# Kernel optimization log

Measured on AMD Instinct MI355X. Metric: run time of the kernel, lower is better.

Reference implementation:

```python
import jax, jax.numpy as jnp
import numpy as np

WS = 8
NUM_HEADS = 8
EMBED_DIM = 256
LN_EPS = 1e-5


def setup_inputs() -> dict:
    key = jax.random.key(0)
    ks = jax.random.split(key, 5)
    b, c, h, w = 4, EMBED_DIM, 128, 128
    return {
        "x": jax.random.normal(ks[0], (b, c, h, w), dtype=jnp.float32),
        "in_proj_w": jax.random.normal(ks[1], (3 * c, c), dtype=jnp.float32) * 0.02,
        "in_proj_b": jax.random.normal(ks[2], (3 * c,), dtype=jnp.float32) * 0.02,
        "out_w": jax.random.normal(ks[3], (c, c), dtype=jnp.float32) * 0.02,
        "out_b": jax.random.normal(ks[4], (c,), dtype=jnp.float32) * 0.02,
        "ln_w": jnp.ones((c,), dtype=jnp.float32),
        "ln_b": jnp.zeros((c,), dtype=jnp.float32),
    }


def reference(x, in_proj_w, in_proj_b, out_w, out_b, ln_w, ln_b):
    b, c, h, w = x.shape
    pad_h = (-h) % WS
    pad_w = (-w) % WS
    xp = jnp.pad(x, ((0, 0), (0, 0), (0, pad_h), (0, pad_w)))
    Hp, Wp = h + pad_h, w + pad_w
    h1, w1 = Hp // WS, Wp // WS
    L = h1 * w1            # attention sequence = number of windows
    N = b * WS * WS        # attention batch = b * within-window positions
    # rearrange 'b c (h1 h2) (w1 w2) -> (h1 w1) (b h2 w2) c', then batch-first
    t = xp.reshape(b, c, h1, WS, w1, WS)
    t = jnp.transpose(t, (2, 4, 0, 3, 5, 1)).reshape(L, N, c)
    t = jnp.transpose(t, (1, 0, 2))  # [N, L, c]
    # nn.MultiheadAttention (self-attention, no mask)
    qkv = t @ in_proj_w.T + in_proj_b  # [N, L, 3c]
    q, k, v = jnp.split(qkv, 3, axis=-1)
    D = c // NUM_HEADS
    q = q.reshape(N, L, NUM_HEADS, D) * (D ** -0.5)
    k = k.reshape(N, L, NUM_HEADS, D)
    v = v.reshape(N, L, NUM_HEADS, D)
    attn = jax.nn.softmax(jnp.einsum('nlhd,nmhd->nhlm', q, k), axis=-1)
    o = jnp.einsum('nhlm,nmhd->nlhd', attn, v).reshape(N, L, c)
    o = o @ out_w.T + out_b
    # LayerNorm over channel dim
    mu = jnp.mean(o, axis=-1, keepdims=True)
    var = jnp.mean(jnp.square(o - mu), axis=-1, keepdims=True)
    o = (o - mu) * jax.lax.rsqrt(var + LN_EPS) * ln_w + ln_b
    # inverse rearrange '(h1 w1) (b h2 w2) c -> b c (h1 h2) (w1 w2)'
    y = jnp.transpose(o, (1, 0, 2)).reshape(h1, w1, b, WS, WS, c)
    y = jnp.transpose(y, (2, 5, 0, 3, 1, 4)).reshape(b, c, Hp, Wp)
    return y[:, :, :h, :w]
```

## Files before the change

kernel.cpp:

```cpp
#include <hip/hip_runtime.h>
#include <stdint.h>
#include <stddef.h>


typedef __attribute__((ext_vector_type(8))) short bf16x8;
typedef __attribute__((ext_vector_type(4))) float f32x4;
typedef __attribute__((ext_vector_type(16))) float f32x16;
typedef __attribute__((ext_vector_type(4))) unsigned u32x4;
typedef __attribute__((ext_vector_type(2))) unsigned u32x2;
typedef unsigned short bf16u;

#define LOG2E 1.4426950408889634f
#define MFMA32(a, b, c) __builtin_amdgcn_mfma_f32_32x32x16_bf16(a, b, c, 0, 0, 0)

__device__ __forceinline__ bf16u f2b(float f) {
  uint32_t u = __float_as_uint(f);
  u += 0x7fffu + ((u >> 16) & 1u);
  return (bf16u)(u >> 16);
}
__device__ __forceinline__ float b2f(bf16u s) {
  return __uint_as_float(((uint32_t)s) << 16);
}

__device__ __forceinline__ void gload_lds16(const void* g, void* l) {
  __builtin_amdgcn_global_load_lds((__attribute__((address_space(1))) void*)(g),
                                   (__attribute__((address_space(3))) void*)(l),
                                   16, 0, 0);
}

__device__ __forceinline__ unsigned cvtpk(float a, float b) {
  unsigned r;
  asm("v_cvt_pk_bf16_f32 %0, %1, %2" : "=v"(r) : "v"(a), "v"(b));
  return r;
}

__device__ __forceinline__ void swap32(unsigned a, unsigned b, bool hi,
                                       unsigned& x, unsigned& y) {
#if __has_builtin(__builtin_amdgcn_permlane32_swap)
  typedef __attribute__((ext_vector_type(2))) unsigned uint2v;
  uint2v r = __builtin_amdgcn_permlane32_swap(a, b, false, false);
  x = r.x;
  y = r.y;
#else
  unsigned as = (unsigned)__shfl_xor((int)a, 32);
  unsigned bs = (unsigned)__shfl_xor((int)b, 32);
  x = hi ? bs : a;
  y = hi ? b : as;
#endif
}

__global__ __launch_bounds__(256) void k_convert(const float* __restrict__ s,
                                                 bf16u* __restrict__ d, int n) {
  int i = blockIdx.x * 256 + threadIdx.x;
  if (i < n) d[i] = f2b(s[i]);
}

__global__ __launch_bounds__(256) void k_rearrange(const float* __restrict__ x,
                                                   bf16u* __restrict__ Tb) {
  const int bid = blockIdx.x;
  const int ct = bid & 7, hh = (bid >> 3) & 127, b = bid >> 10;
  const int c0 = ct * 32;
  const int h1 = hh >> 3, h2 = hh & 7;
  __shared__ float tile[32][129];
  for (int e = threadIdx.x; e < 4096; e += 256) {
    int cc = e >> 7, ww = e & 127;
    tile[cc][ww] = x[(((size_t)(b * 256 + c0 + cc)) * 128 + hh) * 128 + ww];
  }
  __syncthreads();
  for (int e = threadIdx.x; e < 4096; e += 256) {
    int ww = e >> 5, cc = e & 31;
    int w1 = ww >> 3, w2 = ww & 7;
    int i = ((b * 64 + h2 * 8 + w2) << 8) | (h1 * 16 + w1);
    Tb[(size_t)i * 256 + c0 + cc] = f2b(tile[cc][ww]);
  }
}

__global__ __launch_bounds__(256) void k_qkv(const bf16u* __restrict__ Tb,
                                             const bf16u* __restrict__ Wb,
                                             const float* __restrict__ bias,
                                             bf16u* __restrict__ Qb,
                                             bf16u* __restrict__ Kb,
                                             bf16u* __restrict__ Vtb) {
  __shared__ bf16u As[128 * 64];
  __shared__ bf16u Bs[128 * 64];
  const int bid0 = blockIdx.x;
  const int bid = (bid0 & 7) * 384 + (bid0 >> 3);
  const int o0 = (bid % 6) * 128;
  const int i0 = (bid / 6) * 128;
  const int seg = o0 >> 8;
  const int t = threadIdx.x;
  const int lane = t & 63, lo = lane & 15, hi = lane >> 4;
  const int w = t >> 6, wr = w >> 1, wc = w & 1;
  const int rr = t >> 3, cc8 = t & 7;
  f32x4 acc[4][4] = {};
  for (int k0 = 0; k0 < 256; k0 += 64) {
    __syncthreads();
#pragma unroll
    for (int j = 0; j < 4; ++j) {
      const int row = j * 32 + rr;
      const int sc = (cc8 ^ (row & 7)) * 8;
      bf16u* const da = As + (j * 32 + w * 8) * 64;
      bf16u* const db = Bs + (j * 32 + w * 8) * 64;
      gload_lds16(Tb + (size_t)(i0 + row) * 256 + k0 + sc, da);
      gload_lds16(Wb + (size_t)(o0 + row) * 256 + k0 + sc, db);
    }
    __syncthreads();
#pragma unroll
    for (int ks = 0; ks < 2; ++ks) {
      bf16x8 af[4], bf_[4];
#pragma unroll
      for (int m = 0; m < 4; ++m) {
        const int row = wr * 64 + m * 16 + lo;
        const int c = (ks * 4 + hi) ^ (lo & 7);
        af[m] = *(const bf16x8*)&As[row * 64 + c * 8];
      }
#pragma unroll
      for (int nn = 0; nn < 4; ++nn) {
        const int row = wc * 64 + nn * 16 + lo;
        const int c = (ks * 4 + hi) ^ (lo & 7);
        bf_[nn] = *(const bf16x8*)&Bs[row * 64 + c * 8];
      }
#pragma unroll
      for (int m = 0; m < 4; ++m)
#pragma unroll
        for (int nn = 0; nn < 4; ++nn)
          acc[m][nn] = __builtin_amdgcn_mfma_f32_16x16x32_bf16(af[m], bf_[nn], acc[m][nn], 0, 0, 0);
    }
  }
  const float oscale = (seg == 0) ? (0.17677669529663687f * LOG2E) : 1.0f;
#pragma unroll
  for (int m = 0; m < 4; ++m) {
#pragma unroll
    for (int nn = 0; nn < 4; ++nn) {
      const int o = o0 + wc * 64 + nn * 16 + lo;
      const int within = o & 255, head = within >> 5, dd = within & 31;
      const float bia = bias[o];
      const int tok0 = i0 + wr * 64 + m * 16 + hi * 4;
      const int nt = tok0 >> 8, ls0 = tok0 & 255;
      if (seg == 2) {
        float v0 = acc[m][nn][0] + bia, v1 = acc[m][nn][1] + bia;
        float v2 = acc[m][nn][2] + bia, v3 = acc[m][nn][3] + bia;
        u32x2 pkd = {cvtpk(v0, v1), cvtpk(v2, v3)};
        *(u32x2*)(Vtb + ((size_t)((nt * 8 + head) * 32 + dd)) * 256 + ls0) = pkd;
      } else {
        bf16u* const dst = (seg == 0) ? Qb : Kb;
#pragma unroll
        for (int r = 0; r < 4; ++r) {
          float v = (acc[m][nn][r] + bia) * oscale;
          dst[((size_t)((nt * 8 + head) * 256 + ls0 + r)) * 32 + dd] = f2b(v);
        }
      }
    }
  }
}

__global__ __launch_bounds__(256, 2) void k_attn(const bf16u* __restrict__ Qb,
                                                 const bf16u* __restrict__ Kb,
                                                 const bf16u* __restrict__ Vtb,
                                                 bf16u* __restrict__ Ob) {
  const int nh = blockIdx.x;
  const int n = nh >> 3, h = nh & 7;
  const bf16u* Qp = Qb + (size_t)nh * 8192;
  const bf16u* Kp = Kb + (size_t)nh * 8192;
  const bf16u* Vp = Vtb + (size_t)nh * 8192;
  const int t = threadIdx.x, w = t >> 6, lane = t & 63;
  const int l31 = lane & 31;
  const bool hi5 = (lane & 32) != 0;

  bf16x8 qf[2][2];
#pragma unroll
  for (int qs = 0; qs < 2; ++qs)
#pragma unroll
    for (int dh = 0; dh < 2; ++dh)
      qf[qs][dh] = *(const bf16x8*)(Qp + (size_t)(w * 64 + qs * 32 + l31) * 32 +
                                    dh * 16 + (hi5 ? 8 : 0));

  const bf16u* kbase = Kp + (size_t)l31 * 32 + (hi5 ? 8 : 0);
  const bf16u* vbase = Vp + (size_t)l31 * 256 + (hi5 ? 8 : 0);

  bf16x8 kf0 = *(const bf16x8*)(kbase);
  bf16x8 kf1 = *(const bf16x8*)(kbase + 16);
  bf16x8 vf0 = *(const bf16x8*)(vbase);
  bf16x8 vf1 = *(const bf16x8*)(vbase + 16);

  f32x16 accO[2] = {};
  float rsum[2] = {0.f, 0.f};

#pragma unroll
  for (int kt = 0; kt < 8; ++kt) {
    const int nkt = (kt + 1) & 7;
    bf16x8 nk0 = *(const bf16x8*)(kbase + nkt * 1024);
    bf16x8 nk1 = *(const bf16x8*)(kbase + nkt * 1024 + 16);
    bf16x8 nv0 = *(const bf16x8*)(vbase + nkt * 32);
    bf16x8 nv1 = *(const bf16x8*)(vbase + nkt * 32 + 16);

#pragma unroll
    for (int qs = 0; qs < 2; ++qs) {
      f32x16 s = {};
      s = MFMA32(kf0, qf[qs][0], s);
      s = MFMA32(kf1, qf[qs][1], s);
      float ts0 = 0.f, ts1 = 0.f;
      unsigned pk[8];
#pragma unroll
      for (int jp = 0; jp < 8; ++jp) {
        float p0 = exp2f(s[2 * jp]);
        float p1 = exp2f(s[2 * jp + 1]);
        ts0 += p0;
        ts1 += p1;
        pk[jp] = cvtpk(p0, p1);
      }
      float ts = ts0 + ts1;
      ts += __shfl_xor(ts, 32);
      rsum[qs] += ts;
      unsigned x0, x1, x2, x3, y0, y1, y2, y3;
      swap32(pk[0], pk[2], hi5, x0, x2);
      swap32(pk[1], pk[3], hi5, x1, x3);
      swap32(pk[4], pk[6], hi5, y0, y2);
      swap32(pk[5], pk[7], hi5, y1, y3);
      u32x4 pa0 = {x0, x1, x2, x3};
      u32x4 pa1 = {y0, y1, y2, y3};
      accO[qs] = MFMA32(__builtin_bit_cast(bf16x8, pa0), vf0, accO[qs]);
      accO[qs] = MFMA32(__builtin_bit_cast(bf16x8, pa1), vf1, accO[qs]);
    }
    kf0 = nk0;
    kf1 = nk1;
    vf0 = nv0;
    vf1 = nv1;
  }
#pragma unroll
  for (int qs = 0; qs < 2; ++qs) {
    float rn = 1.0f / rsum[qs];
#pragma unroll
    for (int r = 0; r < 16; ++r) {
      int row = (r & 3) + 8 * (r >> 2) + ((lane & 32) >> 3);
      float c = __shfl(rn, (lane & 32) | row);
      float o = accO[qs][r] * c;
      Ob[((size_t)(n * 256 + w * 64 + qs * 32 + row)) * 256 + h * 32 + l31] = f2b(o);
    }
  }
}

__global__ __launch_bounds__(256) void k_out(const bf16u* __restrict__ Ob,
                                             const bf16u* __restrict__ Wb,
                                             const float* __restrict__ bias,
                                             const float* __restrict__ lnw,
                                             const float* __restrict__ lnb,
                                             bf16u* __restrict__ On) {
  __shared__ bf16u As[64 * 64];
  __shared__ bf16u Bs[256 * 64];
  __shared__ float red[64][4][2];
  const int i0 = blockIdx.x * 64;
  const int t = threadIdx.x, w = t >> 6, lane = t & 63, lo = lane & 15, hi = lane >> 4;
  const int rr = t >> 3, cc8 = t & 7;
  f32x4 acc[4][4] = {};
  for (int k0 = 0; k0 < 256; k0 += 64) {
    __syncthreads();
#pragma unroll
    for (int j = 0; j < 2; ++j) {
      const int row = j * 32 + rr;
      const int sc = (cc8 ^ (row & 7)) * 8;
      gload_lds16(Ob + (size_t)(i0 + row) * 256 + k0 + sc,
                  As + (j * 32 + w * 8) * 64);
    }
#pragma unroll
    for (int j = 0; j < 8; ++j) {
      const int row = j * 32 + rr;
      const int sc = (cc8 ^ (row & 7)) * 8;
      gload_lds16(Wb + (size_t)row * 256 + k0 + sc,
                  Bs + (j * 32 + w * 8) * 64);
    }
    __syncthreads();
#pragma unroll
    for (int ks = 0; ks < 2; ++ks) {
      bf16x8 af[4], bf_[4];
#pragma unroll
      for (int m = 0; m < 4; ++m) {
        const int row = m * 16 + lo;
        const int c = (ks * 4 + hi) ^ (lo & 7);
        af[m] = *(const bf16x8*)&As[row * 64 + c * 8];
      }
#pragma unroll
      for (int nn = 0; nn < 4; ++nn) {
        const int row = w * 64 + nn * 16 + lo;
        const int c = (ks * 4 + hi) ^ (lo & 7);
        bf_[nn] = *(const bf16x8*)&Bs[row * 64 + c * 8];
      }
#pragma unroll
      for (int m = 0; m < 4; ++m)
#pragma unroll
        for (int nn = 0; nn < 4; ++nn)
          acc[m][nn] = __builtin_amdgcn_mfma_f32_16x16x32_bf16(af[m], bf_[nn], acc[m][nn], 0, 0, 0);
    }
  }
#pragma unroll
  for (int m = 0; m < 4; ++m)
#pragma unroll
    for (int nn = 0; nn < 4; ++nn) {
      float bia = bias[w * 64 + nn * 16 + lo];
#pragma unroll
      for (int r = 0; r < 4; ++r) acc[m][nn][r] += bia;
    }
#pragma unroll
  for (int m = 0; m < 4; ++m)
#pragma unroll
    for (int r = 0; r < 4; ++r) {
      float sv = acc[m][0][r] + acc[m][1][r] + acc[m][2][r] + acc[m][3][r];
      float sq = acc[m][0][r] * acc[m][0][r] + acc[m][1][r] * acc[m][1][r] +
                 acc[m][2][r] * acc[m][2][r] + acc[m][3][r] * acc[m][3][r];
      sv += __shfl_xor(sv, 1); sq += __shfl_xor(sq, 1);
      sv += __shfl_xor(sv, 2); sq += __shfl_xor(sq, 2);
      sv += __shfl_xor(sv, 4); sq += __shfl_xor(sq, 4);
      sv += __shfl_xor(sv, 8); sq += __shfl_xor(sq, 8);
      if (lo == 0) {
        red[m * 16 + hi * 4 + r][w][0] = sv;
        red[m * 16 + hi * 4 + r][w][1] = sq;
      }
    }
  __syncthreads();
#pragma unroll
  for (int m = 0; m < 4; ++m)
#pragma unroll
    for (int r = 0; r < 4; ++r) {
      int row = m * 16 + hi * 4 + r;
      float S  = red[row][0][0] + red[row][1][0] + red[row][2][0] + red[row][3][0];
      float Q2 = red[row][0][1] + red[row][1][1] + red[row][2][1] + red[row][3][1];
      float mu = S * 0.00390625f;
      float var = Q2 * 0.00390625f - mu * mu;
      float rstd = rsqrtf(var + 1e-5f);
#pragma unroll
      for (int nn = 0; nn < 4; ++nn) {
        int oc = w * 64 + nn * 16 + lo;
        float o = (acc[m][nn][r] - mu) * rstd * lnw[oc] + lnb[oc];
        On[(size_t)(i0 + row) * 256 + oc] = f2b(o);
      }
    }
}

__global__ __launch_bounds__(256) void k_unrearrange(const bf16u* __restrict__ On,
                                                     float* __restrict__ y) {
  const int bid = blockIdx.x;
  const int ct = bid & 7, hh = (bid >> 3) & 127, b = bid >> 10;
  const int c0 = ct * 32;
  const int h1 = hh >> 3, h2 = hh & 7;
  __shared__ float tile[32][129];
  for (int e = threadIdx.x; e < 4096; e += 256) {
    int ww = e >> 5, cc = e & 31;
    int w1 = ww >> 3, w2 = ww & 7;
    int i = ((b * 64 + h2 * 8 + w2) << 8) | (h1 * 16 + w1);
    tile[cc][ww] = b2f(On[(size_t)i * 256 + c0 + cc]);
  }
  __syncthreads();
  for (int e = threadIdx.x; e < 4096; e += 256) {
    int cc = e >> 7, ww = e & 127;
    y[(((size_t)(b * 256 + c0 + cc)) * 128 + hh) * 128 + ww] = tile[cc][ww];
  }
}

extern "C" void kernel_launch(void* const* d_in, const int* in_sizes, int n_in,
                              void* d_out, int out_size, void* d_ws, size_t ws_size,
                              hipStream_t stream) {
  const float* x     = (const float*)d_in[0];
  const float* w_qkv = (const float*)d_in[1];
  const float* b_qkv = (const float*)d_in[2];
  const float* w_out = (const float*)d_in[3];
  const float* b_out = (const float*)d_in[4];
  const float* ln_w  = (const float*)d_in[5];
  const float* ln_b  = (const float*)d_in[6];
  float* y = (float*)d_out;

  const size_t SEG = 33554432;
  char* ws = (char*)d_ws;
  if (ws_size < 5 * SEG + 768 * 256 * 2 + 256 * 256 * 2) return;
  bf16u* Tb = (bf16u*)(ws);
  bf16u* Qb = (bf16u*)(ws + SEG);
  bf16u* Kb = (bf16u*)(ws + 2 * SEG);
  bf16u* Vtb = (bf16u*)(ws + 3 * SEG);
  bf16u* Ob = (bf16u*)(ws + 4 * SEG);
  bf16u* Wqkvb = (bf16u*)(ws + 5 * SEG);
  bf16u* Woutb = (bf16u*)(ws + 5 * SEG + 768 * 256 * 2);
  bf16u* On = Tb;

  k_convert<<<768, 256, 0, stream>>>(w_qkv, Wqkvb, 768 * 256);
  k_convert<<<256, 256, 0, stream>>>(w_out, Woutb, 256 * 256);
  k_rearrange<<<4096, 256, 0, stream>>>(x, Tb);
  k_qkv<<<3072, 256, 0, stream>>>(Tb, Wqkvb, b_qkv, Qb, Kb, Vtb);
  k_attn<<<2048, 256, 0, stream>>>(Qb, Kb, Vtb, Ob);
  k_out<<<1024, 256, 0, stream>>>(Ob, Woutb, b_out, ln_w, ln_b, On);
  k_unrearrange<<<4096, 256, 0, stream>>>(On, y);
}
```

Measured before the change: 179.9 us.

## Stage K and V tiles in swizzled LDS for attention kernel

The attention kernel now copies the whole per-head K and V tiles into shared memory with direct global-to-LDS loads and an XOR swizzle, then reads MFMA fragments from LDS. Previously each of the four waves re-read the same K/V fragments from global memory with register double-buffering. The QK MFMAs for both query subtiles are also issued together, with s_setprio raised around the MFMA groups. In exchange the kernel uses 32 KB of LDS per block and adds a barrier, which may limit occupancy and drops the overlap that register prefetching provided.

```diff
diff --git a/kernel.cpp b/kernel.cpp
--- a/kernel.cpp
+++ b/kernel.cpp
@@ -158,6 +158,8 @@
                                                  const bf16u* __restrict__ Kb,
                                                  const bf16u* __restrict__ Vtb,
                                                  bf16u* __restrict__ Ob) {
+  __shared__ bf16u Ks[8192];
+  __shared__ bf16u Vs[8192];
   const int nh = blockIdx.x;
   const int n = nh >> 3, h = nh & 7;
   const bf16u* Qp = Qb + (size_t)nh * 8192;
@@ -166,6 +168,26 @@
   const int t = threadIdx.x, w = t >> 6, lane = t & 63;
   const int l31 = lane & 31;
   const bool hi5 = (lane & 32) != 0;
+  const int hx = hi5 ? 1 : 0;
+
+  const int rr8 = t >> 3, cs8 = t & 7;
+#pragma unroll
+  for (int it = 0; it < 4; ++it) {
+    const int R = it * 32 + rr8;
+    bf16u* const dK = Ks + it * 2048 + (t & 192) * 8;
+    bf16u* const dV = Vs + it * 2048 + (t & 192) * 8;
+    {
+      const int c = cs8 ^ (R & 7);
+      const int kv = (R << 1) | (c >> 2), d0 = (c & 3) << 3;
+      gload_lds16(Kp + (size_t)kv * 32 + d0, dK);
+    }
+    {
+      const int d = R >> 2;
+      const int c = cs8 ^ (d & 7);
+      const int kv0 = ((R & 3) << 6) | (c << 3);
+      gload_lds16(Vp + (size_t)d * 256 + kv0, dV);
+    }
+  }
 
   bf16x8 qf[2][2];
 #pragma unroll
@@ -175,30 +197,37 @@
       qf[qs][dh] = *(const bf16x8*)(Qp + (size_t)(w * 64 + qs * 32 + l31) * 32 +
                                     dh * 16 + (hi5 ? 8 : 0));
 
-  const bf16u* kbase = Kp + (size_t)l31 * 32 + (hi5 ? 8 : 0);
-  const bf16u* vbase = Vp + (size_t)l31 * 256 + (hi5 ? 8 : 0);
-
-  bf16x8 kf0 = *(const bf16x8*)(kbase);
-  bf16x8 kf1 = *(const bf16x8*)(kbase + 16);
-  bf16x8 vf0 = *(const bf16x8*)(vbase);
-  bf16x8 vf1 = *(const bf16x8*)(vbase + 16);
+  __syncthreads();
 
   f32x16 accO[2] = {};
   float rsum[2] = {0.f, 0.f};
+  const f32x16 z = {};
 
 #pragma unroll
   for (int kt = 0; kt < 8; ++kt) {
-    const int nkt = (kt + 1) & 7;
-    bf16x8 nk0 = *(const bf16x8*)(kbase + nkt * 1024);
-    bf16x8 nk1 = *(const bf16x8*)(kbase + nkt * 1024 + 16);
-    bf16x8 nv0 = *(const bf16x8*)(vbase + nkt * 32);
-    bf16x8 nv1 = *(const bf16x8*)(vbase + nkt * 32 + 16);
+    const int kvb = kt * 32;
+    const int kvr = kvb + l31, Rk = kvr >> 1, pre = (kvr & 1) << 2;
+    const int cs0 = (pre | hx) ^ (Rk & 7);
+    const int cs1 = (pre | (2 + hx)) ^ (Rk & 7);
+    bf16x8 kf0 = *(const bf16x8*)&Ks[Rk * 64 + cs0 * 8];
+    bf16x8 kf1 = *(const bf16x8*)&Ks[Rk * 64 + cs1 * 8];
+    const int kv0 = kvb + hx * 8;
+    const int Rv0 = (l31 << 2) | (kv0 >> 6), cv0 = ((kv0 & 63) >> 3) ^ (l31 & 7);
+    const int kv1 = kv0 + 16;
+    const int Rv1 = (l31 << 2) | (kv1 >> 6), cv1 = ((kv1 & 63) >> 3) ^ (l31 & 7);
+    bf16x8 vf0 = *(const bf16x8*)&Vs[Rv0 * 64 + cv0 * 8];
+    bf16x8 vf1 = *(const bf16x8*)&Vs[Rv1 * 64 + cv1 * 8];
+
+    __builtin_amdgcn_s_setprio(1);
+    f32x16 S0 = MFMA32(kf0, qf[0][0], z);
+    S0 = MFMA32(kf1, qf[0][1], S0);
+    f32x16 S1 = MFMA32(kf0, qf[1][0], z);
+    S1 = MFMA32(kf1, qf[1][1], S1);
+    __builtin_amdgcn_s_setprio(0);
 
 #pragma unroll
     for (int qs = 0; qs < 2; ++qs) {
-      f32x16 s = {};
-      s = MFMA32(kf0, qf[qs][0], s);
-      s = MFMA32(kf1, qf[qs][1], s);
+      const f32x16 s = qs == 0 ? S0 : S1;
       float ts0 = 0.f, ts1 = 0.f;
       unsigned pk[8];
 #pragma unroll
@@ -219,13 +248,11 @@
       swap32(pk[5], pk[7], hi5, y1, y3);
       u32x4 pa0 = {x0, x1, x2, x3};
       u32x4 pa1 = {y0, y1, y2, y3};
+      __builtin_amdgcn_s_setprio(1);
       accO[qs] = MFMA32(__builtin_bit_cast(bf16x8, pa0), vf0, accO[qs]);
       accO[qs] = MFMA32(__builtin_bit_cast(bf16x8, pa1), vf1, accO[qs]);
-    }
-    kf0 = nk0;
-    kf1 = nk1;
-    vf0 = nv0;
-    vf1 = nv1;
+      __builtin_amdgcn_s_setprio(0);
+    }
   }
 #pragma unroll
   for (int qs = 0; qs < 2; ++qs) {
```

Measured after the change: 183.9 us. +2.2%, slower.
